# Performance work log

Measured on AMD Instinct MI355X. Metric: run time of the kernel, lower is better.

The kernel has to match this reference:

```python
import jax, jax.numpy as jnp
import numpy as np

B, CIN, CNECK, COUT = 8, 128, 128, 256
NV, NF = 10242, 20480  # icosphere level 5: nv = 10*4^5+2, nf = 20*4^5
EPS = 1e-5


def spmatmul(x, rows, cols, vals, m):
    # x: [..., N]; out[..., r] += vals[k] * x[..., cols[k]] for rows[k] == r
    g = x[..., cols] * vals
    return jnp.zeros(x.shape[:-1] + (m,), x.dtype).at[..., rows].add(g)


def conv1x1(x, w, b):
    # x: [B, Cin, N], w: [Cout, Cin], b: [Cout]
    return jnp.einsum('oi,bin->bon', w, x) + b[None, :, None]


def batchnorm1d(x, gamma, beta):
    # training-mode BN over (batch, spatial) per channel, biased variance
    mean = jnp.mean(x, axis=(0, 2), keepdims=True)
    var = jnp.var(x, axis=(0, 2), keepdims=True)
    xhat = (x - mean) * jax.lax.rsqrt(var + EPS)
    return gamma[None, :, None] * xhat + beta[None, :, None]


def setup_inputs() -> dict:
    key = jax.random.key(0)
    ks = jax.random.split(key, 16)

    def coo(k, nrows, per_row, ncols, scale):
        rows = jnp.repeat(jnp.arange(nrows, dtype=jnp.int32), per_row)
        cols = jax.random.randint(k, (nrows * per_row,), 0, ncols, dtype=jnp.int32)
        vals = jax.random.normal(jax.random.fold_in(k, 1), (nrows * per_row,), jnp.float32) * scale
        return rows, cols, vals

    Gr, Gc, Gv = coo(ks[0], 3 * NF, 3, NV, 0.5)
    Lr, Lc, Lv = coo(ks[1], NV, 7, NV, 0.3)
    Fr, Fc, Fv = coo(ks[2], NV, 6, NF, 1.0 / 6.0)

    def nrm(k, shape, scale=1.0):
        return jax.random.normal(k, shape, jnp.float32) * scale

    s_in = 1.0 / np.sqrt(CIN)
    s_nk = 1.0 / np.sqrt(CNECK)
    s_cf = 1.0 / np.sqrt(4 * CNECK)
    return {
        'x': nrm(ks[3], (B, CIN, NV)),
        'w1a': nrm(ks[4], (CNECK, CIN), s_in), 'b1a': nrm(ks[5], (CNECK,), s_in),
        'g1a': jnp.ones((CNECK,), jnp.float32), 'be1a': jnp.zeros((CNECK,), jnp.float32),
        'coeffs': nrm(ks[6], (CNECK * 4, CNECK), s_cf),
        'g2a': jnp.ones((CNECK,), jnp.float32), 'be2a': jnp.zeros((CNECK,), jnp.float32),
        'w3a': nrm(ks[7], (COUT, CNECK), s_nk), 'b3a': nrm(ks[8], (COUT,), s_nk),
        'g3a': jnp.ones((COUT,), jnp.float32), 'be3a': jnp.zeros((COUT,), jnp.float32),
        'w1b': nrm(ks[9], (COUT, CIN), s_in), 'b1b': nrm(ks[10], (COUT,), s_in),
        'g1b': jnp.ones((COUT,), jnp.float32), 'be1b': jnp.zeros((COUT,), jnp.float32),
        'G_vals': Gv, 'L_vals': Lv, 'F2V_vals': Fv,
        'EW': nrm(ks[11], (NF, 3)), 'NS': nrm(ks[12], (NF, 3)),
        'G_rows': Gr, 'G_cols': Gc,
        'L_rows': Lr, 'L_cols': Lc,
        'F2V_rows': Fr, 'F2V_cols': Fc,
    }


def mesh_conv(h, coeffs, G_rows, G_cols, G_vals, L_rows, L_cols, L_vals,
              F2V_rows, F2V_cols, F2V_vals, EW, NS):
    b, c, nv = h.shape
    # gradient on faces: [B,C,3*NF] -> [B,C,3,NF] -> [B,C,NF,3]
    grad_face = spmatmul(h, G_rows, G_cols, G_vals, 3 * NF)
    grad_face = grad_face.reshape(b, c, 3, NF).transpose(0, 1, 3, 2)
    laplacian = spmatmul(h, L_rows, L_cols, L_vals, NV)
    identity = h  # stride=1 => nv_prev == nv
    gf_ew = jnp.sum(grad_face * EW, axis=-1)  # [B,C,NF]
    gf_ns = jnp.sum(grad_face * NS, axis=-1)
    gv_ew = spmatmul(gf_ew, F2V_rows, F2V_cols, F2V_vals, NV)
    gv_ns = spmatmul(gf_ns, F2V_rows, F2V_cols, F2V_vals, NV)
    feat = jnp.stack([identity, laplacian, gv_ew, gv_ns], axis=-1)  # [B,C,NV,4]
    # [B,NV,C*4] @ [C*4,Cout] -> [B,Cout,NV]  (note: no bias added in original forward)
    out = jnp.matmul(feat.transpose(0, 2, 1, 3).reshape(b, nv, c * 4), coeffs)
    return out.transpose(0, 2, 1)


def reference(x, w1a, b1a, g1a, be1a, coeffs, g2a, be2a, w3a, b3a, g3a, be3a,
              w1b, b1b, g1b, be1b, G_vals, L_vals, F2V_vals, EW, NS,
              G_rows, G_cols, L_rows, L_cols, F2V_rows, F2V_cols):
    # shortcut branch: conv_1b -> bn_1b
    x2 = batchnorm1d(conv1x1(x, w1b, b1b), g1b, be1b)
    # main branch
    h = jax.nn.relu(batchnorm1d(conv1x1(x, w1a, b1a), g1a, be1a))
    h = mesh_conv(h, coeffs, G_rows, G_cols, G_vals, L_rows, L_cols, L_vals,
                  F2V_rows, F2V_cols, F2V_vals, EW, NS)
    h = jax.nn.relu(batchnorm1d(h, g2a, be2a))
    x1 = batchnorm1d(conv1x1(h, w3a, b3a), g3a, be3a)
    return jax.nn.relu(x1 + x2)
```

## Files before the change

kernel.cpp:

```cpp
#include <hip/hip_runtime.h>
#include <math.h>

#define BB   8
#define NVV  10242
#define NFF  20480
#define EPSBN 1e-5f
#define GRAM_BLOCKS 644

typedef __attribute__((ext_vector_type(8))) short bf16x8_t;
typedef __attribute__((ext_vector_type(4))) float f32x4_t;

__device__ inline float bf2f(ushort u) {
    union { uint i; float f; } v; v.i = ((uint)u) << 16; return v.f;
}
__device__ inline ushort f2bf(float f) {
    union { float f; uint i; } v; v.f = f;
    const uint r = v.i + 0x7fffu + ((v.i >> 16) & 1u);
    return (ushort)(r >> 16);
}
__device__ inline void unpack2(uint w, float& lo, float& hi) {
    union { uint i; float f; } a, b;
    a.i = w << 16; b.i = w & 0xffff0000u;
    lo = a.f; hi = b.f;
}
__device__ inline uint pack2(float lo, float hi) {
    return (uint)f2bf(lo) | ((uint)f2bf(hi) << 16);
}
__device__ inline void fma8(const uint4 hv, const float w, float s[8]) {
    float lo, hi;
    unpack2(hv.x, lo, hi); s[0] = fmaf(w, lo, s[0]); s[1] = fmaf(w, hi, s[1]);
    unpack2(hv.y, lo, hi); s[2] = fmaf(w, lo, s[2]); s[3] = fmaf(w, hi, s[3]);
    unpack2(hv.z, lo, hi); s[4] = fmaf(w, lo, s[4]); s[5] = fmaf(w, hi, s[5]);
    unpack2(hv.w, lo, hi); s[6] = fmaf(w, lo, s[6]); s[7] = fmaf(w, hi, s[7]);
}
__device__ inline uint4 pack8(const float s[8]) {
    uint4 p;
    p.x = pack2(s[0], s[1]); p.y = pack2(s[2], s[3]);
    p.z = pack2(s[4], s[5]); p.w = pack2(s[6], s[7]);
    return p;
}

__global__ __launch_bounds__(256)
void gram_kernel(const float* __restrict__ x, float* __restrict__ gramPart,
                 float* __restrict__ xsumPart, uint* __restrict__ xTu)
{
    __shared__ __align__(16) ushort Ahi[128 * 64];
    __shared__ __align__(16) ushort Alo[128 * 64];
    const int t = threadIdx.x;
    const int l = t & 63, wid = t >> 6;
    const int l15 = l & 15, l4 = l >> 4;
    f32x4_t acc[2][8];
#pragma unroll
    for (int m = 0; m < 2; ++m)
#pragma unroll
        for (int n = 0; n < 8; ++n) acc[m][n] = (f32x4_t){0.f, 0.f, 0.f, 0.f};
    float xs[8] = {0.f, 0.f, 0.f, 0.f, 0.f, 0.f, 0.f, 0.f};

    for (int s = 0; s < 2; ++s) {
        const int cc = blockIdx.x * 2 + s;
        const int b = cc / 161, tb = cc % 161, v0 = tb * 64;
#pragma unroll
        for (int i = 0; i < 8; ++i) {
            const int item = t + (i << 8);
            const int c = item >> 4, vq = item & 15;
            const int gv = v0 + (vq << 2);
            const float* xp = x + ((size_t)b * 128 + c) * NVV + gv;
            float4 xv = make_float4(0.f, 0.f, 0.f, 0.f);
            if (gv + 4 <= NVV) {
                xv = *reinterpret_cast<const float4*>(xp);
            } else {
                if (gv     < NVV) xv.x = xp[0];
                if (gv + 1 < NVV) xv.y = xp[1];
// ... 113 lines not shown
    const float invN = 1.f / (float)(BB * NVV);
    const bool isA = cc < 128;
    const int c = isA ? cc : cc - 128;
    const float* Wrow = isA ? (w1a + (size_t)c * 128) : (w1b + (size_t)c * 128);
    __shared__ float Wr[128];
    __shared__ float red[4];
    Wr[t] = Wrow[t];
    __syncthreads();
    float gi = 0.f;
    const float* Grow = Gram + (size_t)t * 128;
    for (int j = 0; j < 128; ++j) gi = fmaf(Grow[j], Wr[j], gi);
    float pi = Wr[t] * gi * invN;
    float qi = (xsum[t] * invN) * Wr[t];
    for (int off = 32; off > 0; off >>= 1) {
        pi += __shfl_down(pi, off);
        qi += __shfl_down(qi, off);
    }
    const int wid = t >> 6;
    if ((t & 63) == 0) { red[wid] = pi; red[2 + wid] = qi; }
    __syncthreads();
    if (t == 0) {
        const float P = red[0] + red[1], Q = red[2] + red[3];
        const float var = P - Q * Q;
        const float g = isA ? g1a[c] : g1b[c];
        const float be = isA ? be1a[c] : be1b[c];
        const float a = g * rsqrtf(var + EPSBN);
        if (isA) { alpha_a[c] = a; beta_a[c] = be - a * Q; }
        else     { alpha_b[c] = a; beta_b[c] = be - a * Q; }
    }
}

__global__ __launch_bounds__(256)
void prepack_weights_kernel(const float* __restrict__ w1a, const float* __restrict__ w1b,
                            const float* __restrict__ w3a, uint* __restrict__ wpk)
{
    const int j = blockIdx.x * 256 + threadIdx.x;
    const int seg = j >> 12;
    const int slab = seg >> 1, kc = (seg & 1) << 6;
    const int u = j & 4095;
    const int o = u >> 5;
    const int inner = (u << 2) & 127;
    const int inner0 = inner ^ ((o & 7) << 4);
    const int kp = inner0 >> 2;
    const float* W;
    if (slab == 0)      W = w1a;
    else if (slab <= 2) W = w1b + (size_t)(slab - 1) * 128 * 128;
    else                W = w3a + (size_t)(slab - 3) * 128 * 128;
    const float2 wv = *reinterpret_cast<const float2*>(&W[(size_t)o * 128 + kc + 2 * kp]);
    wpk[j] = pack2(wv.x, wv.y);
}

template <int MODE>
__global__ __launch_bounds__(256)
void mfma_conv_kernel(const ushort* __restrict__ Asrc, const uint4* __restrict__ wpk,
                      const float* __restrict__ aIn, const float* __restrict__ bIn,
                      const float* __restrict__ aA, const float* __restrict__ bA,
                      const float* __restrict__ aB, const float* __restrict__ bB,
                      ushort* __restrict__ hOut, ushort* __restrict__ x2Out,
                      ushort* __restrict__ x1Out,
                      float* __restrict__ statSum, float* __restrict__ statSsq)
{
    __shared__ __align__(16) ushort As[128 * 128];
    __shared__ __align__(16) ushort Bs[128 * 64];
    __shared__ float statS[256], statQ[256];
    const int t = threadIdx.x;
    const int bid = blockIdx.x;
    const int b = bid & 7, vblk = bid >> 3;
    const int v0 = vblk * 128;
    const int l = t & 63, wid = t >> 6;
    const int wr = wid >> 1, wc = wid & 1;
    const int l15 = l & 15, l4 = l >> 4;

#pragma unroll
    for (int i = 0; i < 8; ++i) {
        const int item = t + (i << 8);
        const int r = item >> 4, piece = item & 15;
        const int cb = piece * 8;
        const int v = v0 + r;
        uint4 pk = make_uint4(0u, 0u, 0u, 0u);
        if (v < NVV) {
            pk = *reinterpret_cast<const uint4*>(Asrc + ((size_t)b * NVV + v) * 128 + cb);
            if (MODE == 1) {
                float s[8];
                unpack2(pk.x, s[0], s[1]); unpack2(pk.y, s[2], s[3]);
                unpack2(pk.z, s[4], s[5]); unpack2(pk.w, s[6], s[7]);
                const float4 a0 = *reinterpret_cast<const float4*>(&aIn[cb]);
                const float4 a1 = *reinterpret_cast<const float4*>(&aIn[cb + 4]);
                const float4 b0 = *reinterpret_cast<const float4*>(&bIn[cb]);
                const float4 b1 = *reinterpret_cast<const float4*>(&bIn[cb + 4]);
                s[0] = fmaxf(fmaf(a0.x, s[0], b0.x), 0.f);
                s[1] = fmaxf(fmaf(a0.y, s[1], b0.y), 0.f);
                s[2] = fmaxf(fmaf(a0.z, s[2], b0.z), 0.f);
                s[3] = fmaxf(fmaf(a0.w, s[3], b0.w), 0.f);
                s[4] = fmaxf(fmaf(a1.x, s[4], b1.x), 0.f);
                s[5] = fmaxf(fmaf(a1.y, s[5], b1.y), 0.f);
                s[6] = fmaxf(fmaf(a1.z, s[6], b1.z), 0.f);
                s[7] = fmaxf(fmaf(a1.w, s[7], b1.w), 0.f);
                pk = pack8(s);
            }
        }
        const int byte = (r << 8) + (piece << 4);
        *reinterpret_cast<uint4*>((char*)As + (byte ^ ((r & 7) << 4))) = pk;
    }

    const int NZ = (MODE == 0) ? 3 : 2;
    for (int z = 0; z < NZ; ++z) {
        const int slab = (MODE == 0) ? z : (3 + z);
        f32x4_t acc[4][4];
#pragma unroll
        for (int m = 0; m < 4; ++m)
#pragma unroll
            for (int n = 0; n < 4; ++n) acc[m][n] = (f32x4_t){0.f, 0.f, 0.f, 0.f};

        for (int kc = 0; kc < 128; kc += 64) {
            const uint4* wseg = wpk + (size_t)(slab * 2 + (kc >> 6)) * 1024;
#pragma unroll
            for (int i = 0; i < 4; ++i)
                reinterpret_cast<uint4*>(Bs)[t + (i << 8)] = wseg[t + (i << 8)];
            __syncthreads();
#pragma unroll
            for (int kk2 = 0; kk2 < 2; ++kk2) {
                bf16x8_t af[4], bfr[4];
#pragma unroll
                for (int m = 0; m < 4; ++m) {
                    const int row = wr * 64 + m * 16 + l15;
                    const int byte = (row << 8) + (kc << 1) + (kk2 << 6) + (l4 << 4);
                    af[m] = *reinterpret_cast<const bf16x8_t*>((const char*)As + (byte ^ ((row & 7) << 4)));
                }
#pragma unroll
                for (int n = 0; n < 4; ++n) {
                    const int o = wc * 64 + n * 16 + l15;
                    const int byte = (o << 7) + (kk2 << 6) + (l4 << 4);
                    bfr[n] = *reinterpret_cast<const bf16x8_t*>((const char*)Bs + (byte ^ ((o & 7) << 4)));
                }
#pragma unroll
                for (int m = 0; m < 4; ++m)
#pragma unroll
                    for (int n = 0; n < 4; ++n)
                        acc[m][n] = __builtin_amdgcn_mfma_f32_16x16x32_bf16(af[m], bfr[n], acc[m][n], 0, 0, 0);
            }
            __syncthreads();
        }

        if (MODE == 0 && z == 0) {
            float aO[4], bO[4];
#pragma unroll
            for (int n = 0; n < 4; ++n) {
                const int c = wc * 64 + n * 16 + l15;
                aO[n] = aA[c]; bO[n] = bA[c];
            }
#pragma unroll
            for (int m = 0; m < 4; ++m) {
#pragma unroll
                for (int j = 0; j < 4; ++j) {
                    const int v = v0 + wr * 64 + m * 16 + l4 * 4 + j;
                    if (v < NVV) {
                        ushort* mp = hOut + ((size_t)b * NVV + v) * 128 + wc * 64 + l15;
#pragma unroll
                        for (int n = 0; n < 4; ++n)
                            mp[n * 16] = f2bf(fmaxf(fmaf(aO[n], acc[m][n][j], bO[n]), 0.f));
                    }
                }
            }
        } else if (MODE == 0) {
            float aO[4], bO[4];
#pragma unroll
            for (int n = 0; n < 4; ++n) {
                const int cl = wc * 64 + n * 16 + l15;
                aO[n] = aB[(z - 1) * 128 + cl]; bO[n] = bB[(z - 1) * 128 + cl];
            }
#pragma unroll
            for (int m = 0; m < 4; ++m) {
                const int vbase = v0 + wr * 64 + m * 16 + l4 * 4;
#pragma unroll
                for (int n = 0; n < 4; ++n) {
                    const int cl = wc * 64 + n * 16 + l15;
                    const int ch = (z - 1) * 128 + cl;
                    ushort* p = x2Out + ((size_t)b * 256 + ch) * NVV + vbase;
                    if (vbase + 4 <= NVV) {
                        uint* pu = (uint*)p;
                        pu[0] = pack2(fmaf(aO[n], acc[m][n][0], bO[n]),
                                      fmaf(aO[n], acc[m][n][1], bO[n]));
                        pu[1] = pack2(fmaf(aO[n], acc[m][n][2], bO[n]),
                                      fmaf(aO[n], acc[m][n][3], bO[n]));
                    } else {
#pragma unroll
                        for (int j = 0; j < 4; ++j)
                            if (vbase + j < NVV)
                                p[j] = f2bf(fmaf(aO[n], acc[m][n][j], bO[n]));
                    }
                }
            }
        } else {
            float ss[4] = {0.f, 0.f, 0.f, 0.f}, sq[4] = {0.f, 0.f, 0.f, 0.f};
#pragma unroll
            for (int m = 0; m < 4; ++m) {
                const int vbase = v0 + wr * 64 + m * 16 + l4 * 4;
#pragma unroll
                for (int n = 0; n < 4; ++n) {
                    const int cl = wc * 64 + n * 16 + l15;
                    const int ch = z * 128 + cl;
                    ushort* p = x1Out + ((size_t)b * 256 + ch) * NVV + vbase;
                    if (vbase + 4 <= NVV) {
                        float v0f = acc[m][n][0], v1f = acc[m][n][1];
                        float v2f = acc[m][n][2], v3f = acc[m][n][3];
                        uint* pu = (uint*)p;
                        pu[0] = pack2(v0f, v1f);
                        pu[1] = pack2(v2f, v3f);
                        ss[n] += v0f + v1f + v2f + v3f;
                        sq[n] = fmaf(v0f, v0f, sq[n]); sq[n] = fmaf(v1f, v1f, sq[n]);
                        sq[n] = fmaf(v2f, v2f, sq[n]); sq[n] = fmaf(v3f, v3f, sq[n]);
                    } else {
#pragma unroll
                        for (int j = 0; j < 4; ++j) {
                            if (vbase + j < NVV) {
                                const float val = acc[m][n][j];
                                p[j] = f2bf(val);
                                ss[n] += val;
                                sq[n] = fmaf(val, val, sq[n]);
                            }
                        }
                    }
                }
            }
#pragma unroll
            for (int n = 0; n < 4; ++n) {
                ss[n] += __shfl_xor(ss[n], 16); ss[n] += __shfl_xor(ss[n], 32);
                sq[n] += __shfl_xor(sq[n], 16); sq[n] += __shfl_xor(sq[n], 32);
            }
            if (l < 16) {
#pragma unroll
                for (int n = 0; n < 4; ++n) {
                    statS[wr * 128 + wc * 64 + n * 16 + l] = ss[n];
                    statQ[wr * 128 + wc * 64 + n * 16 + l] = sq[n];
                }
            }
            __syncthreads();
            if (t < 128) {
                const int slot = b * 81 + vblk;
                statSum[((size_t)z * 648 + slot) * 128 + t] = statS[t] + statS[128 + t];
                statSsq[((size_t)z * 648 + slot) * 128 + t] = statQ[t] + statQ[128 + t];
            }
            __syncthreads();
        }
    }
}

__global__ __launch_bounds__(256)
void face_kernel(const ushort* __restrict__ h, const float* __restrict__ Gv,
                 const int* __restrict__ Gc, const float* __restrict__ EW,
                 const float* __restrict__ NSm, ushort* __restrict__ gf)
{
    const int t = threadIdx.x;
    const int lane = t & 63, wid = t >> 6;
    const int bid = blockIdx.x;
    const int b = bid & 7;
    const int f = (bid >> 3) * 4 + wid;
    const uint* hb = (const uint*)h + (size_t)b * NVV * 64;
    float ewx = 0.f, ewy = 0.f, nsx = 0.f, nsy = 0.f;
#pragma unroll
    for (int e = 0; e < 3; ++e) {
        const size_t r3 = ((size_t)e * NFF + f) * 3;
        float gx = 0.f, gy = 0.f;
#pragma unroll
        for (int j = 0; j < 3; ++j) {
            const float w = Gv[r3 + j];
            const int col = Gc[r3 + j];
            const uint hv = hb[(size_t)col * 64 + lane];
            float lo, hi; unpack2(hv, lo, hi);
            gx = fmaf(w, lo, gx); gy = fmaf(w, hi, gy);
        }
        const float we = EW[f * 3 + e], wn = NSm[f * 3 + e];
        ewx = fmaf(we, gx, ewx); ewy = fmaf(we, gy, ewy);
        nsx = fmaf(wn, gx, nsx); nsy = fmaf(wn, gy, nsy);
    }
    uint* go = (uint*)gf + ((size_t)b * NFF + f) * 128;
    go[lane]      = pack2(ewx, ewy);
    go[64 + lane] = pack2(nsx, nsy);
}

__global__ __launch_bounds__(256)
void prepack_coeffs_kernel(const float* __restrict__ coeffs, uint* __restrict__ cpk)
{
    const int j = blockIdx.x * 256 + threadIdx.x;
    const int chunk = j >> 12, u = j & 4095;
    const int o = u >> 5;
    const int inner = (u << 2) & 127;
    const int inner0 = inner ^ ((o & 7) << 4);
    const int p = inner0 >> 2;
    const int q = chunk >> 1, c0 = (chunk & 1) << 6;
    const int row0 = (c0 + 2 * p) * 4 + q;
    cpk[j] = pack2(coeffs[(size_t)row0 * 128 + o], coeffs[(size_t)(row0 + 4) * 128 + o]);
}

__global__ __launch_bounds__(512)
void mesh_gemm_kernel(const ushort* __restrict__ h, const ushort* __restrict__ gf,
                      const uint4* __restrict__ cpk,
                      const float* __restrict__ Lv, const int* __restrict__ Lc,
                      const float* __restrict__ Fv, const int* __restrict__ Fc,
                      ushort* __restrict__ meshraw,
                      float* __restrict__ msum, float* __restrict__ mssq)
{
    __shared__ __align__(16) ushort As[128 * 64];
    __shared__ __align__(16) ushort Bs[128 * 64];
    __shared__ float statS[512], statQ[512];
    __shared__ int   LciS[896];
    __shared__ float LwS[896];
    __shared__ int   FciS[768];
    __shared__ float FwS[768];
    const int t = threadIdx.x;
    const int bid = blockIdx.x;
    const int b = bid & 7;
    const int vblk = bid >> 3;
    const int v0 = vblk * 128;
    const int l = t & 63, wid = t >> 6;
    const int wr = wid >> 1, wc = wid & 1;
    const int l15 = l & 15, l4 = l >> 4;
    const size_t hb = (size_t)b * NVV * 128;

    for (int i = t; i < 896; i += 512) {
        const int g = v0 * 7 + i;
        if (g < NVV * 7) { LciS[i] = Lc[g]; LwS[i] = Lv[g]; }
    }
    for (int i = t; i < 768; i += 512) {
        const int g = v0 * 6 + i;
        if (g < NVV * 6) { FciS[i] = Fc[g]; FwS[i] = Fv[g]; }
    }
    __syncthreads();

    f32x4_t acc[2][4];
#pragma unroll
    for (int m = 0; m < 2; ++m)
#pragma unroll
        for (int n = 0; n < 4; ++n) acc[m][n] = (f32x4_t){0.f, 0.f, 0.f, 0.f};

    for (int chunk = 0; chunk < 8; ++chunk) {
        const int q = chunk >> 1, c0 = (chunk & 1) << 6;
#pragma unroll
        for (int i = 0; i < 2; ++i) {
            const int item = t + (i << 9);
            const int r = item >> 3, piece = item & 7;
            const int cb = c0 + piece * 8;
            const int v = v0 + r;
            uint4 pk = make_uint4(0u, 0u, 0u, 0u);
            if (v < NVV) {
                if (q == 0) {
                    pk = *reinterpret_cast<const uint4*>(h + hb + (size_t)v * 128 + cb);
                } else if (q == 1) {
                    float s[8] = {0.f, 0.f, 0.f, 0.f, 0.f, 0.f, 0.f, 0.f};
#pragma unroll
                    for (int j = 0; j < 7; ++j) {
                        const float w = LwS[r * 7 + j];
                        const int col = LciS[r * 7 + j];
                        const uint4 hv = *reinterpret_cast<const uint4*>(h + hb + (size_t)col * 128 + cb);
                        fma8(hv, w, s);
                    }
                    pk = pack8(s);
                } else {
                    const int slab = q - 2;
                    float s[8] = {0.f, 0.f, 0.f, 0.f, 0.f, 0.f, 0.f, 0.f};
#pragma unroll
                    for (int j = 0; j < 6; ++j) {
                        const float w = FwS[r * 6 + j];
                        const int f = FciS[r * 6 + j];
                        const uint4 gv = *reinterpret_cast<const uint4*>(
                            gf + (((size_t)b * NFF + f) * 2 + slab) * 128 + cb);
                        fma8(gv, w, s);
                    }
                    pk = pack8(s);
                }
            }
            const int byte = (r << 7) + (piece << 4);
            *reinterpret_cast<uint4*>((char*)As + (byte ^ ((r & 7) << 4))) = pk;
        }
#pragma unroll
        for (int i = 0; i < 2; ++i) {
            const int idx = t + (i << 9);
            reinterpret_cast<uint4*>(Bs)[idx] = cpk[chunk * 1024 + idx];
        }
        __syncthreads();
#pragma unroll
        for (int kk2 = 0; kk2 < 2; ++kk2) {
            bf16x8_t af[2], bfr[4];
#pragma unroll
            for (int m = 0; m < 2; ++m) {
                const int row = wr * 32 + m * 16 + l15;
                const int byte = (row << 7) + (kk2 << 6) + (l4 << 4);
                af[m] = *reinterpret_cast<const bf16x8_t*>((const char*)As + (byte ^ ((row & 7) << 4)));
            }
#pragma unroll
            for (int n = 0; n < 4; ++n) {
                const int o = wc * 64 + n * 16 + l15;
                const int byte = (o << 7) + (kk2 << 6) + (l4 << 4);
                bfr[n] = *reinterpret_cast<const bf16x8_t*>((const char*)Bs + (byte ^ ((o & 7) << 4)));
            }
#pragma unroll
            for (int m = 0; m < 2; ++m)
#pragma unroll
                for (int n = 0; n < 4; ++n)
                    acc[m][n] = __builtin_amdgcn_mfma_f32_16x16x32_bf16(af[m], bfr[n], acc[m][n], 0, 0, 0);
        }
        __syncthreads();
    }
    float ss[4] = {0.f, 0.f, 0.f, 0.f}, sq[4] = {0.f, 0.f, 0.f, 0.f};
#pragma unroll
    for (int m = 0; m < 2; ++m) {
#pragma unroll
        for (int j = 0; j < 4; ++j) {
            const int row = wr * 32 + m * 16 + l4 * 4 + j;
            const int v = v0 + row;
            if (v < NVV) {
                ushort* mp = meshraw + hb + (size_t)v * 128 + wc * 64 + l15;
#pragma unroll
                for (int n = 0; n < 4; ++n) {
                    const float val = acc[m][n][j];
                    mp[n * 16] = f2bf(val);
                    ss[n] += val;
                    sq[n] = fmaf(val, val, sq[n]);
                }
            }
        }
    }
#pragma unroll
    for (int n = 0; n < 4; ++n) {
        ss[n] += __shfl_xor(ss[n], 16); ss[n] += __shfl_xor(ss[n], 32);
        sq[n] += __shfl_xor(sq[n], 16); sq[n] += __shfl_xor(sq[n], 32);
    }
    if (l < 16) {
#pragma unroll
        for (int n = 0; n < 4; ++n) {
            statS[wr * 128 + wc * 64 + n * 16 + l] = ss[n];
            statQ[wr * 128 + wc * 64 + n * 16 + l] = sq[n];
        }
    }
    __syncthreads();
    if (t < 128) {
        const int blk = b * 81 + vblk;
        msum[(size_t)blk * 128 + t] = statS[t] + statS[128 + t] + statS[256 + t] + statS[384 + t];
        mssq[(size_t)blk * 128 + t] = statQ[t] + statQ[128 + t] + statQ[256 + t] + statQ[384 + t];
    }
}

__global__ __launch_bounds__(256)
void finalize_stats_kernel(const float* __restrict__ s, const float* __restrict__ q, int count,
                           const float* __restrict__ g, const float* __restrict__ be,
                           float* __restrict__ alpha, float* __restrict__ beta, int split)
{
    const int c = blockIdx.x, t = threadIdx.x;
    const size_t base = split ? ((size_t)(c >> 7) * count * 128 + (c & 127)) : (size_t)c;
    float ls = 0.f, lq = 0.f;
    for (int i = t; i < count; i += 256) {
        ls += s[base + (size_t)i * 128];
        lq += q[base + (size_t)i * 128];
    }
    __shared__ float rs[256], rq[256];
    rs[t] = ls; rq[t] = lq;
    __syncthreads();
    for (int off = 128; off > 0; off >>= 1) {
        if (t < off) { rs[t] += rs[t + off]; rq[t] += rq[t + off]; }
        __syncthreads();
    }
    if (t == 0) {
        const float invN = 1.f / (float)(BB * NVV);
        const float mean = rs[0] * invN;
        const float var = rq[0] * invN - mean * mean;
        const float a = g[c] * rsqrtf(var + EPSBN);
        alpha[c] = a;
        beta[c] = be[c] - a * mean;
    }
}
// ... 30 lines not shown
    const float* coeffs = (const float*)d_in[5];
    const float* g2a    = (const float*)d_in[6];
    const float* be2a   = (const float*)d_in[7];
    const float* w3a    = (const float*)d_in[8];
    const float* g3a    = (const float*)d_in[10];
    const float* be3a   = (const float*)d_in[11];
    const float* w1b    = (const float*)d_in[12];
    const float* g1b    = (const float*)d_in[14];
    const float* be1b   = (const float*)d_in[15];
    const float* Gv     = (const float*)d_in[16];
    const float* Lv     = (const float*)d_in[17];
    const float* Fv     = (const float*)d_in[18];
    const float* EW     = (const float*)d_in[19];
    const float* NSm    = (const float*)d_in[20];
    const int*   Gc     = (const int*)d_in[22];
    const int*   Lc     = (const int*)d_in[24];
    const int*   Fc     = (const int*)d_in[26];

    char* base = (char*)d_ws;
    size_t off = 0;
    auto alloc = [&](size_t bytes) { char* p = base + off; off += (bytes + 255) & ~(size_t)255; return p; };

    const size_t gfBytes = (size_t)BB * NFF * 2 * 128 * 2;
    char* region0   = alloc(gfBytes);
    float* gramPart = (float*)region0;
    float* xsumPart = (float*)(region0 + (size_t)GRAM_BLOCKS * 16384 * 4);
    ushort* gf      = (ushort*)region0;
    ushort* x1      = (ushort*)region0;

    ushort* xT      = (ushort*)alloc((size_t)BB * NVV * 128 * 2);
    ushort* h       = (ushort*)alloc((size_t)BB * NVV * 128 * 2);
    ushort* meshraw = (ushort*)alloc((size_t)BB * NVV * 128 * 2);
    ushort* x2      = (ushort*)alloc((size_t)BB * 256 * NVV * 2);
    uint*  cpk      = (uint*)alloc(32768 * 4);
    uint*  wpk      = (uint*)alloc(40960 * 4);
    float* Gram     = (float*)alloc(16384 * 4);
    float* xsum     = (float*)alloc(128 * 4);
    float* alpha_a  = (float*)alloc(128 * 4);
    float* beta_a   = (float*)alloc(128 * 4);
    float* alpha_b  = (float*)alloc(256 * 4);
    float* beta_b   = (float*)alloc(256 * 4);
    float* alpha2   = (float*)alloc(128 * 4);
    float* beta2    = (float*)alloc(128 * 4);
    float* alpha3   = (float*)alloc(256 * 4);
    float* beta3    = (float*)alloc(256 * 4);
    float* msum     = (float*)alloc((size_t)648 * 128 * 4);
    float* mssq     = (float*)alloc((size_t)648 * 128 * 4);
    float* x1sum    = (float*)alloc((size_t)2 * 648 * 128 * 4);
    float* x1ssq    = (float*)alloc((size_t)2 * 648 * 128 * 4);
    if (off > ws_size) return;

    gram_kernel<<<GRAM_BLOCKS, 256, 0, stream>>>(x, gramPart, xsumPart, (uint*)xT);
    reduce_gram_kernel<<<64, 256, 0, stream>>>(gramPart, xsumPart, Gram, xsum);
    stats_ab_kernel<<<384, 128, 0, stream>>>(Gram, xsum, w1a, g1a, be1a, w1b, g1b, be1b,
                                             alpha_a, beta_a, alpha_b, beta_b);
    prepack_coeffs_kernel<<<128, 256, 0, stream>>>(coeffs, cpk);
    prepack_weights_kernel<<<160, 256, 0, stream>>>(w1a, w1b, w3a, wpk);
    mfma_conv_kernel<0><<<648, 256, 0, stream>>>(
        xT, (const uint4*)wpk, nullptr, nullptr, alpha_a, beta_a, alpha_b, beta_b,
        h, x2, nullptr, nullptr, nullptr);
    face_kernel<<<(NFF / 4) * 8, 256, 0, stream>>>(h, Gv, Gc, EW, NSm, gf);
    mesh_gemm_kernel<<<648, 512, 0, stream>>>(h, gf, (const uint4*)cpk,
                                              Lv, Lc, Fv, Fc, meshraw, msum, mssq);
    finalize_stats_kernel<<<128, 256, 0, stream>>>(msum, mssq, 648, g2a, be2a, alpha2, beta2, 0);
    mfma_conv_kernel<1><<<648, 256, 0, stream>>>(
        meshraw, (const uint4*)wpk, alpha2, beta2, nullptr, nullptr, nullptr, nullptr,
        nullptr, nullptr, x1, x1sum, x1ssq);
    finalize_stats_kernel<<<256, 256, 0, stream>>>(x1sum, x1ssq, 648, g3a, be3a, alpha3, beta3, 1);
    final_kernel<<<2048, 256, 0, stream>>>((float*)d_out, x1, x2, alpha3, beta3);
}
```

Baseline: 316.7 us.

## Drop LDS staging in conv and mesh GEMMs, split output slabs across blocks

The 1x1 conv kernels no longer stage activations and weights in shared memory. Each lane loads its MFMA fragments straight from global memory using plain bf16 row-major weights, and the output slabs are spread across the grid (3x or 2x more blocks) instead of looped inside one block. The mesh GEMM is rebuilt in the same way: 256-thread blocks, 1288 blocks, operands gathered directly into registers, coefficients read from a simple chunked bf16 layout. This removes LDS traffic and barriers and raises parallelism, but the activation rows are now re-read from global or L2 once per slab block, and the weight reads are not swizzled.

```diff
diff --git a/kernel.cpp b/kernel.cpp
--- a/kernel.cpp
+++ b/kernel.cpp
@@ -38,6 +38,9 @@
     p.x = pack2(s[0], s[1]); p.y = pack2(s[2], s[3]);
     p.z = pack2(s[4], s[5]); p.w = pack2(s[6], s[7]);
     return p;
+}
+__device__ inline bf16x8_t as_bf8(uint4 u) {
+    union { uint4 q; bf16x8_t b; } c; c.q = u; return c.b;
 }
 
 __global__ __launch_bounds__(256)
@@ -217,216 +220,203 @@
 
 __global__ __launch_bounds__(256)
 void prepack_weights_kernel(const float* __restrict__ w1a, const float* __restrict__ w1b,
-                            const float* __restrict__ w3a, uint* __restrict__ wpk)
+                            const float* __restrict__ w3a, ushort* __restrict__ wpku)
 {
     const int j = blockIdx.x * 256 + threadIdx.x;
-    const int seg = j >> 12;
-    const int slab = seg >> 1, kc = (seg & 1) << 6;
-    const int u = j & 4095;
-    const int o = u >> 5;
-    const int inner = (u << 2) & 127;
-    const int inner0 = inner ^ ((o & 7) << 4);
-    const int kp = inner0 >> 2;
+    if (j >= 5 * 16384) return;
+    const int slab = j >> 14, rem = j & 16383;
     const float* W;
     if (slab == 0)      W = w1a;
     else if (slab <= 2) W = w1b + (size_t)(slab - 1) * 128 * 128;
     else                W = w3a + (size_t)(slab - 3) * 128 * 128;
-    const float2 wv = *reinterpret_cast<const float2*>(&W[(size_t)o * 128 + kc + 2 * kp]);
-    wpk[j] = pack2(wv.x, wv.y);
+    wpku[j] = f2bf(W[rem]);
+}
+
+__global__ __launch_bounds__(256)
+void prepack_coeffs_kernel(const float* __restrict__ coeffs, ushort* __restrict__ cpku)
+{
+    const int j = blockIdx.x * 256 + threadIdx.x;
+    const int chunk = j >> 13, rem = j & 8191;
+    const int o = rem >> 6, k = rem & 63;
+    const int q = chunk >> 1, ch = chunk & 1;
+    const int row = (ch * 64 + k) * 4 + q;
+    cpku[j] = f2bf(coeffs[(size_t)row * 128 + o]);
 }
 
 template <int MODE>
 __global__ __launch_bounds__(256)
-void mfma_conv_kernel(const ushort* __restrict__ Asrc, const uint4* __restrict__ wpk,
-                      const float* __restrict__ aIn, const float* __restrict__ bIn,
-                      const float* __restrict__ aA, const float* __restrict__ bA,
-                      const float* __restrict__ aB, const float* __restrict__ bB,
-                      ushort* __restrict__ hOut, ushort* __restrict__ x2Out,
-                      ushort* __restrict__ x1Out,
-                      float* __restrict__ statSum, float* __restrict__ statSsq)
-{
-    __shared__ __align__(16) ushort As[128 * 128];
-    __shared__ __align__(16) ushort Bs[128 * 64];
+void conv_kernel(const ushort* __restrict__ Asrc, const ushort* __restrict__ wpku,
+                 const float* __restrict__ aIn, const float* __restrict__ bIn,
+                 const float* __restrict__ aA, const float* __restrict__ bA,
+                 const float* __restrict__ aB, const float* __restrict__ bB,
+                 ushort* __restrict__ hOut, ushort* __restrict__ x2Out,
+                 ushort* __restrict__ x1Out,
+                 float* __restrict__ statSum, float* __restrict__ statSsq)
+{
     __shared__ float statS[256], statQ[256];
+    const int bid = blockIdx.x;
+    const int b = bid & 7;
+    const int rest = bid >> 3;
+    const int vblk = rest % 81, z = rest / 81;
+    const int v0 = vblk * 128;
     const int t = threadIdx.x;
-    const int bid = blockIdx.x;
-    const int b = bid & 7, vblk = bid >> 3;
-    const int v0 = vblk * 128;
     const int l = t & 63, wid = t >> 6;
     const int wr = wid >> 1, wc = wid & 1;
     const int l15 = l & 15, l4 = l >> 4;
-
-#pragma unroll
-    for (int i = 0; i < 8; ++i) {
-        const int item = t + (i << 8);
-        const int r = item >> 4, piece = item & 15;
-        const int cb = piece * 8;
-        const int v = v0 + r;
-        uint4 pk = make_uint4(0u, 0u, 0u, 0u);
-        if (v < NVV) {
-            pk = *reinterpret_cast<const uint4*>(Asrc + ((size_t)b * NVV + v) * 128 + cb);
-            if (MODE == 1) {
-                float s[8];
-                unpack2(pk.x, s[0], s[1]); unpack2(pk.y, s[2], s[3]);
-                unpack2(pk.z, s[4], s[5]); unpack2(pk.w, s[6], s[7]);
-                const float4 a0 = *reinterpret_cast<const float4*>(&aIn[cb]);
-                const float4 a1 = *reinterpret_cast<const float4*>(&aIn[cb + 4]);
-                const float4 b0 = *reinterpret_cast<const float4*>(&bIn[cb]);
-                const float4 b1 = *reinterpret_cast<const float4*>(&bIn[cb + 4]);
-                s[0] = fmaxf(fmaf(a0.x, s[0], b0.x), 0.f);
-                s[1] = fmaxf(fmaf(a0.y, s[1], b0.y), 0.f);
-                s[2] = fmaxf(fmaf(a0.z, s[2], b0.z), 0.f);
-                s[3] = fmaxf(fmaf(a0.w, s[3], b0.w), 0.f);
-                s[4] = fmaxf(fmaf(a1.x, s[4], b1.x), 0.f);
-                s[5] = fmaxf(fmaf(a1.y, s[5], b1.y), 0.f);
-                s[6] = fmaxf(fmaf(a1.z, s[6], b1.z), 0.f);
-                s[7] = fmaxf(fmaf(a1.w, s[7], b1.w), 0.f);
-                pk = pack8(s);
-            }
-        }
-        const int byte = (r << 8) + (piece << 4);
-        *reinterpret_cast<uint4*>((char*)As + (byte ^ ((r & 7) << 4))) = pk;
-    }
-
-    const int NZ = (MODE == 0) ? 3 : 2;
-    for (int z = 0; z < NZ; ++z) {
-        const int slab = (MODE == 0) ? z : (3 + z);
-        f32x4_t acc[4][4];
+    const int slab = (MODE == 0) ? z : (3 + z);
+    const ushort* W = wpku + (size_t)slab * 16384;
+    const ushort* Ab = Asrc + (size_t)b * NVV * 128;
+
+    f32x4_t acc[4][4];
+#pragma unroll
+    for (int m = 0; m < 4; ++m)
+#pragma unroll
+        for (int n = 0; n < 4; ++n) acc[m][n] = (f32x4_t){0.f, 0.f, 0.f, 0.f};
+
+#pragma unroll
+    for (int kq = 0; kq < 4; ++kq) {
+        const int ko = kq * 32 + l4 * 8;
+        bf16x8_t af[4], bfr[4];
+        float4 av0, av1, bv0, bv1;
+        if (MODE == 1) {
+            av0 = *reinterpret_cast<const float4*>(&aIn[ko]);
+            av1 = *reinterpret_cast<const float4*>(&aIn[ko + 4]);
+            bv0 = *reinterpret_cast<const float4*>(&bIn[ko]);
+            bv1 = *reinterpret_cast<const float4*>(&bIn[ko + 4]);
+        }
+#pragma unroll
+        for (int m = 0; m < 4; ++m) {
+            const int v = v0 + wr * 64 + m * 16 + l15;
+            uint4 pk = make_uint4(0u, 0u, 0u, 0u);
+            if (v < NVV) {
+                pk = *reinterpret_cast<const uint4*>(Ab + (size_t)v * 128 + ko);
+                if (MODE == 1) {
+                    float s[8];
+                    unpack2(pk.x, s[0], s[1]); unpack2(pk.y, s[2], s[3]);
+                    unpack2(pk.z, s[4], s[5]); unpack2(pk.w, s[6], s[7]);
+                    s[0] = fmaxf(fmaf(av0.x, s[0], bv0.x), 0.f);
+                    s[1] = fmaxf(fmaf(av0.y, s[1], bv0.y), 0.f);
+                    s[2] = fmaxf(fmaf(av0.z, s[2], bv0.z), 0.f);
+                    s[3] = fmaxf(fmaf(av0.w, s[3], bv0.w), 0.f);
+                    s[4] = fmaxf(fmaf(av1.x, s[4], bv1.x), 0.f);
+                    s[5] = fmaxf(fmaf(av1.y, s[5], bv1.y), 0.f);
+                    s[6] = fmaxf(fmaf(av1.z, s[6], bv1.z), 0.f);
+                    s[7] = fmaxf(fmaf(av1.w, s[7], bv1.w), 0.f);
+                    pk = pack8(s);
+                }
+            }
+            af[m] = as_bf8(pk);
+        }
+#pragma unroll
+        for (int n = 0; n < 4; ++n) {
+            const int o = wc * 64 + n * 16 + l15;
+            bfr[n] = *reinterpret_cast<const bf16x8_t*>(W + (size_t)o * 128 + ko);
+        }
 #pragma unroll
         for (int m = 0; m < 4; ++m)
 #pragma unroll
-            for (int n = 0; n < 4; ++n) acc[m][n] = (f32x4_t){0.f, 0.f, 0.f, 0.f};
-
-        for (int kc = 0; kc < 128; kc += 64) {
-            const uint4* wseg = wpk + (size_t)(slab * 2 + (kc >> 6)) * 1024;
-#pragma unroll
-            for (int i = 0; i < 4; ++i)
-                reinterpret_cast<uint4*>(Bs)[t + (i << 8)] = wseg[t + (i << 8)];
-            __syncthreads();
-#pragma unroll
-            for (int kk2 = 0; kk2 < 2; ++kk2) {
-                bf16x8_t af[4], bfr[4];
-#pragma unroll
-                for (int m = 0; m < 4; ++m) {
-                    const int row = wr * 64 + m * 16 + l15;
-                    const int byte = (row << 8) + (kc << 1) + (kk2 << 6) + (l4 << 4);
-                    af[m] = *reinterpret_cast<const bf16x8_t*>((const char*)As + (byte ^ ((row & 7) << 4)));
-                }
-#pragma unroll
-                for (int n = 0; n < 4; ++n) {
-                    const int o = wc * 64 + n * 16 + l15;
-                    const int byte = (o << 7) + (kk2 << 6) + (l4 << 4);
-                    bfr[n] = *reinterpret_cast<const bf16x8_t*>((const char*)Bs + (byte ^ ((o & 7) << 4)));
-                }
-#pragma unroll
-                for (int m = 0; m < 4; ++m)
+            for (int n = 0; n < 4; ++n)
+                acc[m][n] = __builtin_amdgcn_mfma_f32_16x16x32_bf16(af[m], bfr[n], acc[m][n], 0, 0, 0);
+    }
+
+    if (MODE == 0 && z == 0) {
+        float aO[4], bO[4];
+#pragma unroll
+        for (int n = 0; n < 4; ++n) {
+            const int c = wc * 64 + n * 16 + l15;
+            aO[n] = aA[c]; bO[n] = bA[c];
+        }
+#pragma unroll
+        for (int m = 0; m < 4; ++m) {
+#pragma unroll
+            for (int j = 0; j < 4; ++j) {
+                const int v = v0 + wr * 64 + m * 16 + l4 * 4 + j;
+                if (v < NVV) {
+                    ushort* mp = hOut + ((size_t)b * NVV + v) * 128 + wc * 64 + l15;
 #pragma unroll
                     for (int n = 0; n < 4; ++n)
-                        acc[m][n] = __builtin_amdgcn_mfma_f32_16x16x32_bf16(af[m], bfr[n], acc[m][n], 0, 0, 0);
-            }
-            __syncthreads();
-        }
-
-        if (MODE == 0 && z == 0) {
-            float aO[4], bO[4];
-#pragma unroll
-            for (int n = 0; n < 4; ++n) {
-                const int c = wc * 64 + n * 16 + l15;
-                aO[n] = aA[c]; bO[n] = bA[c];
-            }
-#pragma unroll
-            for (int m = 0; m < 4; ++m) {
-#pragma unroll
-                for (int j = 0; j < 4; ++j) {
-                    const int v = v0 + wr * 64 + m * 16 + l4 * 4 + j;
-                    if (v < NVV) {
-                        ushort* mp = hOut + ((size_t)b * NVV + v) * 128 + wc * 64 + l15;
-#pragma unroll
-                        for (int n = 0; n < 4; ++n)
-                            mp[n * 16] = f2bf(fmaxf(fmaf(aO[n], acc[m][n][j], bO[n]), 0.f));
-                    }
-                }
-            }
-        } else if (MODE == 0) {
-            float aO[4], bO[4];
+                        mp[n * 16] = f2bf(fmaxf(fmaf(aO[n], acc[m][n][j], bO[n]), 0.f));
+                }
+            }
+        }
+    } else if (MODE == 0) {
+        float aO[4], bO[4];
+#pragma unroll
+        for (int n = 0; n < 4; ++n) {
+            const int cl = wc * 64 + n * 16 + l15;
+            aO[n] = aB[(z - 1) * 128 + cl]; bO[n] = bB[(z - 1) * 128 + cl];
+        }
+#pragma unroll
+        for (int m = 0; m < 4; ++m) {
+            const int vbase = v0 + wr * 64 + m * 16 + l4 * 4;
 #pragma unroll
             for (int n = 0; n < 4; ++n) {
                 const int cl = wc * 64 + n * 16 + l15;
-                aO[n] = aB[(z - 1) * 128 + cl]; bO[n] = bB[(z - 1) * 128 + cl];
-            }
-#pragma unroll
-            for (int m = 0; m < 4; ++m) {
-                const int vbase = v0 + wr * 64 + m * 16 + l4 * 4;
-#pragma unroll
-                for (int n = 0; n < 4; ++n) {
-                    const int cl = wc * 64 + n * 16 + l15;
-                    const int ch = (z - 1) * 128 + cl;
-                    ushort* p = x2Out + ((size_t)b * 256 + ch) * NVV + vbase;
-                    if (vbase + 4 <= NVV) {
-                        uint* pu = (uint*)p;
-                        pu[0] = pack2(fmaf(aO[n], acc[m][n][0], bO[n]),
-                                      fmaf(aO[n], acc[m][n][1], bO[n]));
-                        pu[1] = pack2(fmaf(aO[n], acc[m][n][2], bO[n]),
-                                      fmaf(aO[n], acc[m][n][3], bO[n]));
-                    } else {
-#pragma unroll
-                        for (int j = 0; j < 4; ++j)
-                            if (vbase + j < NVV)
-                                p[j] = f2bf(fmaf(aO[n], acc[m][n][j], bO[n]));
-                    }
-                }
-            }
-        } else {
-            float ss[4] = {0.f, 0.f, 0.f, 0.f}, sq[4] = {0.f, 0.f, 0.f, 0.f};
-#pragma unroll
-            for (int m = 0; m < 4; ++m) {
-                const int vbase = v0 + wr * 64 + m * 16 + l4 * 4;
-#pragma unroll
-                for (int n = 0; n < 4; ++n) {
-                    const int cl = wc * 64 + n * 16 + l15;
-                    const int ch = z * 128 + cl;
-                    ushort* p = x1Out + ((size_t)b * 256 + ch) * NVV + vbase;
-                    if (vbase + 4 <= NVV) {
-                        float v0f = acc[m][n][0], v1f = acc[m][n][1];
-                        float v2f = acc[m][n][2], v3f = acc[m][n][3];
-                        uint* pu = (uint*)p;
-                        pu[0] = pack2(v0f, v1f);
-                        pu[1] = pack2(v2f, v3f);
-                        ss[n] += v0f + v1f + v2f + v3f;
-                        sq[n] = fmaf(v0f, v0f, sq[n]); sq[n] = fmaf(v1f, v1f, sq[n]);
-                        sq[n] = fmaf(v2f, v2f, sq[n]); sq[n] = fmaf(v3f, v3f, sq[n]);
-                    } else {
-#pragma unroll
-                        for (int j = 0; j < 4; ++j) {
-                            if (vbase + j < NVV) {
-                                const float val = acc[m][n][j];
-                                p[j] = f2bf(val);
-                                ss[n] += val;
-                                sq[n] = fmaf(val, val, sq[n]);
-                            }
+                const int ch = (z - 1) * 128 + cl;
+                ushort* p = x2Out + ((size_t)b * 256 + ch) * NVV + vbase;
+                if (vbase + 4 <= NVV) {
+                    uint* pu = (uint*)p;
+                    pu[0] = pack2(fmaf(aO[n], acc[m][n][0], bO[n]),
+                                  fmaf(aO[n], acc[m][n][1], bO[n]));
+                    pu[1] = pack2(fmaf(aO[n], acc[m][n][2], bO[n]),
+                                  fmaf(aO[n], acc[m][n][3], bO[n]));
+                } else {
+#pragma unroll
+                    for (int j = 0; j < 4; ++j)
+                        if (vbase + j < NVV)
+                            p[j] = f2bf(fmaf(aO[n], acc[m][n][j], bO[n]));
+                }
+            }
+        }
+    } else {
+        float ss[4] = {0.f, 0.f, 0.f, 0.f}, sq[4] = {0.f, 0.f, 0.f, 0.f};
+#pragma unroll
+        for (int m = 0; m < 4; ++m) {
+            const int vbase = v0 + wr * 64 + m * 16 + l4 * 4;
+#pragma unroll
+            for (int n = 0; n < 4; ++n) {
+                const int cl = wc * 64 + n * 16 + l15;
+                const int ch = z * 128 + cl;
+                ushort* p = x1Out + ((size_t)b * 256 + ch) * NVV + vbase;
+                if (vbase + 4 <= NVV) {
+                    float v0f = acc[m][n][0], v1f = acc[m][n][1];
+                    float v2f = acc[m][n][2], v3f = acc[m][n][3];
+                    uint* pu = (uint*)p;
+                    pu[0] = pack2(v0f, v1f);
+                    pu[1] = pack2(v2f, v3f);
+                    ss[n] += v0f + v1f + v2f + v3f;
+                    sq[n] = fmaf(v0f, v0f, sq[n]); sq[n] = fmaf(v1f, v1f, sq[n]);
+                    sq[n] = fmaf(v2f, v2f, sq[n]); sq[n] = fmaf(v3f, v3f, sq[n]);
+                } else {
+#pragma unroll
+                    for (int j = 0; j < 4; ++j) {
+                        if (vbase + j < NVV) {
+                            const float val = acc[m][n][j];
+                            p[j] = f2bf(val);
+                            ss[n] += val;
+                            sq[n] = fmaf(val, val, sq[n]);
                         }
                     }
                 }
             }
+        }
+#pragma unroll
+        for (int n = 0; n < 4; ++n) {
+            ss[n] += __shfl_xor(ss[n], 16); ss[n] += __shfl_xor(ss[n], 32);
+            sq[n] += __shfl_xor(sq[n], 16); sq[n] += __shfl_xor(sq[n], 32);
+        }
+        if (l < 16) {
 #pragma unroll
             for (int n = 0; n < 4; ++n) {
-                ss[n] += __shfl_xor(ss[n], 16); ss[n] += __shfl_xor(ss[n], 32);
-                sq[n] += __shfl_xor(sq[n], 16); sq[n] += __shfl_xor(sq[n], 32);
-            }
-            if (l < 16) {
-#pragma unroll
-                for (int n = 0; n < 4; ++n) {
-                    statS[wr * 128 + wc * 64 + n * 16 + l] = ss[n];
-                    statQ[wr * 128 + wc * 64 + n * 16 + l] = sq[n];
-                }
-            }
-            __syncthreads();
-            if (t < 128) {
-                const int slot = b * 81 + vblk;
-                statSum[((size_t)z * 648 + slot) * 128 + t] = statS[t] + statS[128 + t];
-                statSsq[((size_t)z * 648 + slot) * 128 + t] = statQ[t] + statQ[128 + t];
-            }
-            __syncthreads();
+                statS[wr * 128 + wc * 64 + n * 16 + l] = ss[n];
+                statQ[wr * 128 + wc * 64 + n * 16 + l] = sq[n];
+            }
+        }
+        __syncthreads();
+        if (t < 128) {
+            const int slot = b * 81 + vblk;
+            statSum[((size_t)z * 648 + slot) * 128 + t] = statS[t] + statS[128 + t];
+            statSsq[((size_t)z * 648 + slot) * 128 + t] = statQ[t] + statQ[128 + t];
         }
     }
 }
@@ -465,162 +455,154 @@
 }
 
 __global__ __launch_bounds__(256)
-void prepack_coeffs_kernel(const float* __restrict__ coeffs, uint* __restrict__ cpk)
-{
-    const int j = blockIdx.x * 256 + threadIdx.x;
-    const int chunk = j >> 12, u = j & 4095;
-    const int o = u >> 5;
-    const int inner = (u << 2) & 127;
-    const int inner0 = inner ^ ((o & 7) << 4);
-    const int p = inner0 >> 2;
-    const int q = chunk >> 1, c0 = (chunk & 1) << 6;
-    const int row0 = (c0 + 2 * p) * 4 + q;
-    cpk[j] = pack2(coeffs[(size_t)row0 * 128 + o], coeffs[(size_t)(row0 + 4) * 128 + o]);
-}
-
-__global__ __launch_bounds__(512)
-void mesh_gemm_kernel(const ushort* __restrict__ h, const ushort* __restrict__ gf,
-                      const uint4* __restrict__ cpk,
-                      const float* __restrict__ Lv, const int* __restrict__ Lc,
-                      const float* __restrict__ Fv, const int* __restrict__ Fc,
-                      ushort* __restrict__ meshraw,
-                      float* __restrict__ msum, float* __restrict__ mssq)
-{
-    __shared__ __align__(16) ushort As[128 * 64];
-    __shared__ __align__(16) ushort Bs[128 * 64];
+void mesh_kernel(const ushort* __restrict__ h, const ushort* __restrict__ gf,
+                 const ushort* __restrict__ cpku,
+                 const float* __restrict__ Lv, const int* __restrict__ Lc,
+                 const float* __restrict__ Fv, const int* __restrict__ Fc,
+                 ushort* __restrict__ meshraw,
+                 float* __restrict__ msum, float* __restrict__ mssq)
+{
+    __shared__ int   LciS[448];
+    __shared__ float LwS[448];
+    __shared__ int   FciS[384];
+    __shared__ float FwS[384];
     __shared__ float statS[512], statQ[512];
-    __shared__ int   LciS[896];
-    __shared__ float LwS[896];
-    __shared__ int   FciS[768];
-    __shared__ float FwS[768];
     const int t = threadIdx.x;
     const int bid = blockIdx.x;
     const int b = bid & 7;
     const int vblk = bid >> 3;
-    const int v0 = vblk * 128;
+    const int v0 = vblk * 64;
     const int l = t & 63, wid = t >> 6;
-    const int wr = wid >> 1, wc = wid & 1;
     const int l15 = l & 15, l4 = l >> 4;
-    const size_t hb = (size_t)b * NVV * 128;
-
-    for (int i = t; i < 896; i += 512) {
+    const ushort* hb = h + (size_t)b * NVV * 128;
+    const ushort* gfb = gf + (size_t)b * NFF * 256;
+
+    for (int i = t; i < 448; i += 256) {
         const int g = v0 * 7 + i;
         if (g < NVV * 7) { LciS[i] = Lc[g]; LwS[i] = Lv[g]; }
     }
-    for (int i = t; i < 768; i += 512) {
+    for (int i = t; i < 384; i += 256) {
         const int g = v0 * 6 + i;
         if (g < NVV * 6) { FciS[i] = Fc[g]; FwS[i] = Fv[g]; }
     }
     __syncthreads();
 
-    f32x4_t acc[2][4];
-#pragma unroll
-    for (int m = 0; m < 2; ++m)
-#pragma unroll
-        for (int n = 0; n < 4; ++n) acc[m][n] = (f32x4_t){0.f, 0.f, 0.f, 0.f};
-
-    for (int chunk = 0; chunk < 8; ++chunk) {
-        const int q = chunk >> 1, c0 = (chunk & 1) << 6;
-#pragma unroll
-        for (int i = 0; i < 2; ++i) {
-            const int item = t + (i << 9);
-            const int r = item >> 3, piece = item & 7;
-            const int cb = c0 + piece * 8;
-            const int v = v0 + r;
-            uint4 pk = make_uint4(0u, 0u, 0u, 0u);
-            if (v < NVV) {
-                if (q == 0) {
-                    pk = *reinterpret_cast<const uint4*>(h + hb + (size_t)v * 128 + cb);
-                } else if (q == 1) {
-                    float s[8] = {0.f, 0.f, 0.f, 0.f, 0.f, 0.f, 0.f, 0.f};
-#pragma unroll
-                    for (int j = 0; j < 7; ++j) {
-                        const float w = LwS[r * 7 + j];
-                        const int col = LciS[r * 7 + j];
-                        const uint4 hv = *reinterpret_cast<const uint4*>(h + hb + (size_t)col * 128 + cb);
-                        fma8(hv, w, s);
-                    }
-                    pk = pack8(s);
-                } else {
-                    const int slab = q - 2;
-                    float s[8] = {0.f, 0.f, 0.f, 0.f, 0.f, 0.f, 0.f, 0.f};
-#pragma unroll
-                    for (int j = 0; j < 6; ++j) {
-                        const float w = FwS[r * 6 + j];
-                        const int f = FciS[r * 6 + j];
-                        const uint4 gv = *reinterpret_cast<const uint4*>(
-                            gf + (((size_t)b * NFF + f) * 2 + slab) * 128 + cb);
-                        fma8(gv, w, s);
-                    }
-                    pk = pack8(s);
-                }
-            }
-            const int byte = (r << 7) + (piece << 4);
-            *reinterpret_cast<uint4*>((char*)As + (byte ^ ((r & 7) << 4))) = pk;
-        }
-#pragma unroll
-        for (int i = 0; i < 2; ++i) {
-            const int idx = t + (i << 9);
-            reinterpret_cast<uint4*>(Bs)[idx] = cpk[chunk * 1024 + idx];
-        }
-        __syncthreads();
+    const int r = wid * 16 + l15;
+    const int v = v0 + r;
+    const bool okv = v < NVV;
+    const ushort* hrow = hb + (size_t)v * 128;
+
+    f32x4_t acc[8];
+#pragma unroll
+    for (int n = 0; n < 8; ++n) acc[n] = (f32x4_t){0.f, 0.f, 0.f, 0.f};
+
+#pragma unroll
+    for (int ch = 0; ch < 2; ++ch) {
+        const int c0 = ch << 6;
+        bf16x8_t a0[2], a1[2];
 #pragma unroll
         for (int kk2 = 0; kk2 < 2; ++kk2) {
-            bf16x8_t af[2], bfr[4];
-#pragma unroll
-            for (int m = 0; m < 2; ++m) {
-                const int row = wr * 32 + m * 16 + l15;
-                const int byte = (row << 7) + (kk2 << 6) + (l4 << 4);
-                af[m] = *reinterpret_cast<const bf16x8_t*>((const char*)As + (byte ^ ((row & 7) << 4)));
-            }
-#pragma unroll
-            for (int n = 0; n < 4; ++n) {
-                const int o = wc * 64 + n * 16 + l15;
-                const int byte = (o << 7) + (kk2 << 6) + (l4 << 4);
-                bfr[n] = *reinterpret_cast<const bf16x8_t*>((const char*)Bs + (byte ^ ((o & 7) << 4)));
-            }
-#pragma unroll
-            for (int m = 0; m < 2; ++m)
-#pragma unroll
-                for (int n = 0; n < 4; ++n)
-                    acc[m][n] = __builtin_amdgcn_mfma_f32_16x16x32_bf16(af[m], bfr[n], acc[m][n], 0, 0, 0);
-        }
-        __syncthreads();
-    }
-    float ss[4] = {0.f, 0.f, 0.f, 0.f}, sq[4] = {0.f, 0.f, 0.f, 0.f};
-#pragma unroll
-    for (int m = 0; m < 2; ++m) {
-#pragma unroll
-        for (int j = 0; j < 4; ++j) {
-            const int row = wr * 32 + m * 16 + l4 * 4 + j;
-            const int v = v0 + row;
-            if (v < NVV) {
-                ushort* mp = meshraw + hb + (size_t)v * 128 + wc * 64 + l15;
-#pragma unroll
-                for (int n = 0; n < 4; ++n) {
-                    const float val = acc[m][n][j];
-                    mp[n * 16] = f2bf(val);
-                    ss[n] += val;
-                    sq[n] = fmaf(val, val, sq[n]);
-                }
-            }
-        }
-    }
-#pragma unroll
-    for (int n = 0; n < 4; ++n) {
+            const int co = c0 + kk2 * 32 + l4 * 8;
+            uint4 p0 = make_uint4(0u, 0u, 0u, 0u);
+            float s[8] = {0.f, 0.f, 0.f, 0.f, 0.f, 0.f, 0.f, 0.f};
+            if (okv) {
+                p0 = *reinterpret_cast<const uint4*>(hrow + co);
+#pragma unroll
+                for (int j = 0; j < 7; ++j) {
+                    const float w = LwS[r * 7 + j];
+                    const int col = LciS[r * 7 + j];
+                    const uint4 hv = *reinterpret_cast<const uint4*>(hb + (size_t)col * 128 + co);
+                    fma8(hv, w, s);
+                }
+            }
+            a0[kk2] = as_bf8(p0);
+            a1[kk2] = as_bf8(pack8(s));
+        }
+        {
+            const int ck0 = (0 * 2 + ch) * 8192, ck1 = (1 * 2 + ch) * 8192;
+#pragma unroll
+            for (int kk2 = 0; kk2 < 2; ++kk2) {
+                const int kof = kk2 * 32 + l4 * 8;
+#pragma unroll
+                for (int n = 0; n < 8; ++n) {
+                    const int o = n * 16 + l15;
+                    const bf16x8_t b0 = *reinterpret_cast<const bf16x8_t*>(cpku + ck0 + o * 64 + kof);
+                    const bf16x8_t b1 = *reinterpret_cast<const bf16x8_t*>(cpku + ck1 + o * 64 + kof);
+                    acc[n] = __builtin_amdgcn_mfma_f32_16x16x32_bf16(a0[kk2], b0, acc[n], 0, 0, 0);
+                    acc[n] = __builtin_amdgcn_mfma_f32_16x16x32_bf16(a1[kk2], b1, acc[n], 0, 0, 0);
+                }
+            }
+        }
+        bf16x8_t a2[2], a3[2];
+#pragma unroll
+        for (int kk2 = 0; kk2 < 2; ++kk2) {
+            const int co = c0 + kk2 * 32 + l4 * 8;
+            float se[8] = {0.f, 0.f, 0.f, 0.f, 0.f, 0.f, 0.f, 0.f};
+            float sn[8] = {0.f, 0.f, 0.f, 0.f, 0.f, 0.f, 0.f, 0.f};
+            if (okv) {
+#pragma unroll
+                for (int j = 0; j < 6; ++j) {
+                    const float w = FwS[r * 6 + j];
+                    const int f = FciS[r * 6 + j];
+                    const ushort* fp = gfb + (size_t)f * 256 + co;
+                    const uint4 ge = *reinterpret_cast<const uint4*>(fp);
+                    const uint4 gn = *reinterpret_cast<const uint4*>(fp + 128);
+                    fma8(ge, w, se);
+                    fma8(gn, w, sn);
+                }
+            }
+            a2[kk2] = as_bf8(pack8(se));
+            a3[kk2] = as_bf8(pack8(sn));
+        }
+        {
+            const int ck2 = (2 * 2 + ch) * 8192, ck3 = (3 * 2 + ch) * 8192;
+#pragma unroll
+            for (int kk2 = 0; kk2 < 2; ++kk2) {
+                const int kof = kk2 * 32 + l4 * 8;
+#pragma unroll
+                for (int n = 0; n < 8; ++n) {
+                    const int o = n * 16 + l15;
+                    const bf16x8_t b2 = *reinterpret_cast<const bf16x8_t*>(cpku + ck2 + o * 64 + kof);
+                    const bf16x8_t b3 = *reinterpret_cast<const bf16x8_t*>(cpku + ck3 + o * 64 + kof);
+                    acc[n] = __builtin_amdgcn_mfma_f32_16x16x32_bf16(a2[kk2], b2, acc[n], 0, 0, 0);
+                    acc[n] = __builtin_amdgcn_mfma_f32_16x16x32_bf16(a3[kk2], b3, acc[n], 0, 0, 0);
+                }
+            }
+        }
+    }
+    float ss[8], sq[8];
+#pragma unroll
+    for (int n = 0; n < 8; ++n) { ss[n] = 0.f; sq[n] = 0.f; }
+#pragma unroll
+    for (int j = 0; j < 4; ++j) {
+        const int row = wid * 16 + l4 * 4 + j;
+        const int vv = v0 + row;
+        if (vv < NVV) {
+            ushort* mp = meshraw + ((size_t)b * NVV + vv) * 128 + l15;
+#pragma unroll
+            for (int n = 0; n < 8; ++n) {
+                const float val = acc[n][j];
+                mp[n * 16] = f2bf(val);
+                ss[n] += val;
+                sq[n] = fmaf(val, val, sq[n]);
+            }
+        }
+    }
+#pragma unroll
+    for (int n = 0; n < 8; ++n) {
         ss[n] += __shfl_xor(ss[n], 16); ss[n] += __shfl_xor(ss[n], 32);
         sq[n] += __shfl_xor(sq[n], 16); sq[n] += __shfl_xor(sq[n], 32);
     }
     if (l < 16) {
 #pragma unroll
-        for (int n = 0; n < 4; ++n) {
-            statS[wr * 128 + wc * 64 + n * 16 + l] = ss[n];
-            statQ[wr * 128 + wc * 64 + n * 16 + l] = sq[n];
+        for (int n = 0; n < 8; ++n) {
+            statS[wid * 128 + n * 16 + l] = ss[n];
+            statQ[wid * 128 + n * 16 + l] = sq[n];
         }
     }
     __syncthreads();
     if (t < 128) {
-        const int blk = b * 81 + vblk;
+        const int blk = b * 161 + vblk;
         msum[(size_t)blk * 128 + t] = statS[t] + statS[128 + t] + statS[256 + t] + statS[384 + t];
         mssq[(size_t)blk * 128 + t] = statQ[t] + statQ[128 + t] + statQ[256 + t] + statQ[384 + t];
     }
@@ -717,8 +699,8 @@
     ushort* h       = (ushort*)alloc((size_t)BB * NVV * 128 * 2);
     ushort* meshraw = (ushort*)alloc((size_t)BB * NVV * 128 * 2);
     ushort* x2      = (ushort*)alloc((size_t)BB * 256 * NVV * 2);
-    uint*  cpk      = (uint*)alloc(32768 * 4);
-    uint*  wpk      = (uint*)alloc(40960 * 4);
+    ushort* cpku    = (ushort*)alloc(65536 * 2);
+    ushort* wpku    = (ushort*)alloc(81920 * 2);
     float* Gram     = (float*)alloc(16384 * 4);
     float* xsum     = (float*)alloc(128 * 4);
     float* alpha_a  = (float*)alloc(128 * 4);
@@ -729,8 +711,8 @@
     float* beta2    = (float*)alloc(128 * 4);
     float* alpha3   = (float*)alloc(256 * 4);
     float* beta3    = (float*)alloc(256 * 4);
-    float* msum     = (float*)alloc((size_t)648 * 128 * 4);
-    float* mssq     = (float*)alloc((size_t)648 * 128 * 4);
+    float* msum     = (float*)alloc((size_t)1288 * 128 * 4);
+    float* mssq     = (float*)alloc((size_t)1288 * 128 * 4);
     float* x1sum    = (float*)alloc((size_t)2 * 648 * 128 * 4);
     float* x1ssq    = (float*)alloc((size_t)2 * 648 * 128 * 4);
     if (off > ws_size) return;
@@ -739,17 +721,17 @@
     reduce_gram_kernel<<<64, 256, 0, stream>>>(gramPart, xsumPart, Gram, xsum);
     stats_ab_kernel<<<384, 128, 0, stream>>>(Gram, xsum, w1a, g1a, be1a, w1b, g1b, be1b,
                                              alpha_a, beta_a, alpha_b, beta_b);
-    prepack_coeffs_kernel<<<128, 256, 0, stream>>>(coeffs, cpk);
-    prepack_weights_kernel<<<160, 256, 0, stream>>>(w1a, w1b, w3a, wpk);
-    mfma_conv_kernel<0><<<648, 256, 0, stream>>>(
-        xT, (const uint4*)wpk, nullptr, nullptr, alpha_a, beta_a, alpha_b, beta_b,
+    prepack_coeffs_kernel<<<256, 256, 0, stream>>>(coeffs, cpku);
+    prepack_weights_kernel<<<320, 256, 0, stream>>>(w1a, w1b, w3a, wpku);
+    conv_kernel<0><<<1944, 256, 0, stream>>>(
+        xT, wpku, nullptr, nullptr, alpha_a, beta_a, alpha_b, beta_b,
         h, x2, nullptr, nullptr, nullptr);
     face_kernel<<<(NFF / 4) * 8, 256, 0, stream>>>(h, Gv, Gc, EW, NSm, gf);
-    mesh_gemm_kernel<<<648, 512, 0, stream>>>(h, gf, (const uint4*)cpk,
-                                              Lv, Lc, Fv, Fc, meshraw, msum, mssq);
-    finalize_stats_kernel<<<128, 256, 0, stream>>>(msum, mssq, 648, g2a, be2a, alpha2, beta2, 0);
-    mfma_conv_kernel<1><<<648, 256, 0, stream>>>(
-        meshraw, (const uint4*)wpk, alpha2, beta2, nullptr, nullptr, nullptr, nullptr,
+    mesh_kernel<<<1288, 256, 0, stream>>>(h, gf, cpku, Lv, Lc, Fv, Fc,
+                                          meshraw, msum, mssq);
+    finalize_stats_kernel<<<128, 256, 0, stream>>>(msum, mssq, 1288, g2a, be2a, alpha2, beta2, 0);
+    conv_kernel<1><<<1296, 256, 0, stream>>>(
+        meshraw, wpku, alpha2, beta2, nullptr, nullptr, nullptr, nullptr,
         nullptr, nullptr, x1, x1sum, x1ssq);
     finalize_stats_kernel<<<256, 256, 0, stream>>>(x1sum, x1ssq, 648, g3a, be3a, alpha3, beta3, 1);
     final_kernel<<<2048, 256, 0, stream>>>((float*)d_out, x1, x2, alpha3, beta3);
```

New measurement: 423.6 us. 33.7% more time.
